# Optimization experiments

Measured on AMD Instinct MI355X. Metric: run time of the kernel, lower is better.

Reference implementation:

```python
import jax, jax.numpy as jnp
import numpy as np

B, S, D = 1, 1024, 4096
NH, NKV, HD = 32, 8, 128
CACHE = 1024


def setup_inputs() -> dict:
    key = jax.random.key(0)
    ks = jax.random.split(key, 9)
    return {
        "hidden_states": jax.random.normal(ks[0], (B, S, D), jnp.float32),
        "freqs_cos": jax.random.uniform(ks[1], (S, HD // 2), jnp.float32),
        "freqs_sin": jax.random.uniform(ks[2], (S, HD // 2), jnp.float32),
        "atten_mask": jnp.zeros((S, CACHE + S), jnp.float32),
        "k_cache": jax.random.normal(ks[3], (B, NKV, HD, CACHE), jnp.float32),
        "v_cache": jax.random.normal(ks[4], (B, NKV, CACHE, HD), jnp.float32),
        "wq": jax.random.normal(ks[5], (NH, HD, D), jnp.float32) * 0.02,
        "wk": jax.random.normal(ks[6], (NKV, HD, D), jnp.float32) * 0.02,
        "wv": jax.random.normal(ks[7], (NKV, HD, D), jnp.float32) * 0.02,
        "wo": jax.random.normal(ks[8], (D, NH * HD), jnp.float32) * 0.02,
    }


def _rope(x, cos, sin):
    # x: [b, s, h, hd]; cos/sin: [s, hd//2]
    half = x.shape[-1] // 2
    xr, xi = x[..., :half], x[..., half:]
    c = cos[None, :, None, :]
    sn = sin[None, :, None, :]
    return jnp.concatenate([xr * c - xi * sn, xr * sn + xi * c], axis=-1)


def reference(hidden_states, freqs_cos, freqs_sin, atten_mask, k_cache, v_cache, wq, wk, wv, wo):
    b, s, d = hidden_states.shape
    nh, hd, _ = wq.shape
    nkv = wk.shape[0]
    g = nh // nkv  # query heads per KV head
    scale = float(hd) ** 0.5

    # projections (equivalent to per-head 1x1 convs)
    q = jnp.einsum("bsd,hed->bshe", hidden_states, wq)   # [b,s,nh,hd]
    k = jnp.einsum("bsd,hed->bshe", hidden_states, wk)   # [b,s,nkv,hd]
    v = jnp.einsum("bsd,hed->bshe", hidden_states, wv)   # [b,s,nkv,hd]

    q = _rope(q, freqs_cos, freqs_sin)
    k = _rope(k, freqs_cos, freqs_sin)

    # concat KV cache: kh [b,nkv,hd,KV], vh [b,nkv,KV,hd]
    kh = jnp.concatenate([k_cache, k.transpose(0, 2, 3, 1)], axis=-1)
    vh = jnp.concatenate([v_cache, v.transpose(0, 2, 1, 3)], axis=2)

    # grouped attention: head i uses kv group i // g
    qg = q.reshape(b, s, nkv, g, hd).transpose(0, 2, 3, 1, 4)  # [b,n,g,s,e]
    scores = jnp.einsum("bngse,bnet->bngst", qg, kh) / scale + atten_mask
    p = jax.nn.softmax(scores, axis=-1)
    yg = jnp.einsum("bngst,bnte->bngse", p, vh)               # [b,n,g,s,e]
    y = yg.transpose(0, 3, 1, 2, 4).reshape(b, s, nh * hd)     # head order n*g+j

    y = jnp.einsum("bsf,df->bsd", y, wo)
    return (y, kh, vh)
```

## Files before the change

kernel.cpp:

```cpp
#include <hip/hip_runtime.h>
#include <hip/hip_bf16.h>
#include <stdint.h>

#define S_LEN 1024
#define D_MODEL 4096
#define NHEAD 32
#define NKV 8
#define HD 128
#define CACHE_T 1024
#define T_TOT 2048
#define NQKV 6144
#define QSCALE 0.08838834764831845f

typedef __attribute__((ext_vector_type(8))) short short8;
typedef __attribute__((ext_vector_type(4))) float floatx4;
typedef __attribute__((ext_vector_type(16))) float floatx16;

__device__ __forceinline__ unsigned short f2bf(float f) {
  union { float f; uint32_t u; } v; v.f = f;
  uint32_t r = v.u + 0x7FFFu + ((v.u >> 16) & 1u);
  return (unsigned short)(r >> 16);
}

__device__ __forceinline__ unsigned pack2bf(float a, float b) {
  union { __hip_bfloat162 h2; unsigned u; } c;
  c.h2 = __float22bfloat162_rn(make_float2(a, b));
  return c.u;
}

__device__ __forceinline__ void gload_lds16(const void* g, void* s) {
  __builtin_amdgcn_global_load_lds((const __attribute__((address_space(1))) void*)g,
                                   (__attribute__((address_space(3))) void*)s, 16, 0, 0);
}

__global__ void convf2b_kernel(const float* __restrict__ in, unsigned short* __restrict__ out, int n8) {
  int stride = gridDim.x * blockDim.x;
  for (int t = blockIdx.x * blockDim.x + threadIdx.x; t < n8; t += stride) {
    int i = t * 8;
    floatx4 a = *(const floatx4*)(in + i);
    floatx4 b = *(const floatx4*)(in + i + 4);
    short8 o;
    o[0] = (short)f2bf(a[0]); o[1] = (short)f2bf(a[1]); o[2] = (short)f2bf(a[2]); o[3] = (short)f2bf(a[3]);
    o[4] = (short)f2bf(b[0]); o[5] = (short)f2bf(b[1]); o[6] = (short)f2bf(b[2]); o[7] = (short)f2bf(b[3]);
    *(short8*)(out + i) = o;
  }
}

__global__ void mask_flag_kernel(const float* __restrict__ m, int n, int* __restrict__ flag) {
  int stride = gridDim.x * blockDim.x;
  bool nz = false;
  for (int i = blockIdx.x * blockDim.x + threadIdx.x; i < n; i += stride)
    nz |= (m[i] != 0.0f);
  if (nz) atomicOr(flag, 1);
}

__global__ __launch_bounds__(256, 3)
void gemm_bf_kernel(const unsigned short* __restrict__ A,
                    const unsigned short* __restrict__ W,
                    float* __restrict__ C,
                    int M, int N, int K, int ldc, int GM)
{
  __shared__ __align__(16) unsigned char As[2][64 * 128];
  __shared__ __align__(16) unsigned char Bs[2][128 * 128];

  const int nwg = gridDim.x;
  int orig = blockIdx.x;
  int wg = (orig & 7) * (nwg >> 3) + (orig >> 3);
  const int mt = wg % GM, nt = wg / GM;
  const int m0 = mt * 64, n0 = nt * 128;

  const int tid = threadIdx.x;
  const int wid = tid >> 6, lane = tid & 63;
  const int g4 = lane >> 4, r16 = lane & 15;
  const int wr = (wid >> 1) * 32, wc = (wid & 1) * 64;

  const int lr = lane >> 3, lc = lane & 7;
  const unsigned short* Arow[2];
  const unsigned short* Wrow[4];
#pragma unroll
  for (int i = 0; i < 2; ++i) {
    int r = (wid * 2 + i) * 8 + lr;
    Arow[i] = A + (size_t)(m0 + r) * K + (lc ^ (r & 7)) * 8;
  }
#pragma unroll
  for (int i = 0; i < 4; ++i) {
    int r = (wid * 4 + i) * 8 + lr;
    Wrow[i] = W + (size_t)(n0 + r) * K + (lc ^ (r & 7)) * 8;
  }

  auto stage = [&](int buf, int kt) {
    const int kb = kt * 64;
#pragma unroll
    for (int i = 0; i < 2; ++i)
      gload_lds16(Arow[i] + kb, &As[buf][(wid * 2 + i) * 1024]);
#pragma unroll
    for (int i = 0; i < 4; ++i)
      gload_lds16(Wrow[i] + kb, &Bs[buf][(wid * 4 + i) * 1024]);
  };

  floatx4 acc[2][4];
#pragma unroll
  for (int m = 0; m < 2; ++m)
#pragma unroll
    for (int n = 0; n < 4; ++n) acc[m][n] = (floatx4){0.f, 0.f, 0.f, 0.f};

  const int NK = K >> 6;
  stage(0, 0);
  __syncthreads();
  int cur = 0;
  for (int kt = 0; kt < NK; ++kt) {
    if (kt + 1 < NK) stage(cur ^ 1, kt + 1);
#pragma unroll
    for (int kk = 0; kk < 2; ++kk) {
      const int kb = kk * 64 + g4 * 16;
      short8 af[2], bf[4];
#pragma unroll
      for (int m = 0; m < 2; ++m) {
        int row = wr + m * 16 + r16;
        af[m] = *(const short8*)(&As[cur][row * 128 + (kb ^ ((row & 7) << 4))]);
      }
#pragma unroll
      for (int n = 0; n < 4; ++n) {
        int row = wc + n * 16 + r16;
        bf[n] = *(const short8*)(&Bs[cur][row * 128 + (kb ^ ((row & 7) << 4))]);
      }
#pragma unroll
      for (int m = 0; m < 2; ++m)
#pragma unroll
        for (int n = 0; n < 4; ++n)
          acc[m][n] = __builtin_amdgcn_mfma_f32_16x16x32_bf16(af[m], bf[n], acc[m][n], 0, 0, 0);
    }
    __syncthreads();
    cur ^= 1;
  }

#pragma unroll
  for (int m = 0; m < 2; ++m)
#pragma unroll
    for (int n = 0; n < 4; ++n)
#pragma unroll
      for (int j = 0; j < 4; ++j)
        C[(size_t)(m0 + wr + m * 16 + g4 * 4 + j) * ldc + (n0 + wc + n * 16 + r16)] = acc[m][n][j];
}

__global__ __launch_bounds__(256, 2)
void gemm_kernel(const unsigned short* __restrict__ A,
                 const float* __restrict__ W0, const float* __restrict__ W1, const float* __restrict__ W2,
                 int n1, int n2,
                 float* __restrict__ C,
                 int M, int N, int K, int GM)
{
  __shared__ __align__(16) unsigned char As[2][128 * 128];
  __shared__ __align__(16) unsigned char Bs[2][128 * 128];

  const int nwg = gridDim.x;
  int orig = blockIdx.x;
  int xcd = orig & 7, loc = orig >> 3;
  int q = nwg >> 3, r = nwg & 7;
  int wg = (xcd < r ? xcd * (q + 1) : r * (q + 1) + (xcd - r) * q) + loc;
  const int mt = wg % GM, nt = wg / GM;
  const int m0 = mt * 128, n0 = nt * 128;

  const int tid = threadIdx.x;
  const int wid = tid >> 6, lane = tid & 63;
  const int g4 = lane >> 4, r16 = lane & 15;
  const int wr = (wid >> 1) * 64, wc = (wid & 1) * 64;

  int srow[4], skc[4];
  const float* wptr[4];
#pragma unroll
  for (int i = 0; i < 4; ++i) {
    int c = tid + 256 * i;
    srow[i] = c >> 3; skc[i] = c & 7;
    int ng = n0 + srow[i];
    wptr[i] = (ng < n1) ? (W0 + (size_t)ng * K)
            : (ng < n2) ? (W1 + (size_t)(ng - n1) * K)
                        : (W2 + (size_t)(ng - n2) * K);
  }

  short8 ar[4]; floatx4 br[8];
  auto load_tile = [&](int kt) {
    int kb = kt * 64;
#pragma unroll
    for (int i = 0; i < 4; ++i) {
      ar[i] = *(const short8*)(A + (size_t)(m0 + srow[i]) * K + kb + skc[i] * 8);
      br[2 * i]     = *(const floatx4*)(wptr[i] + kb + skc[i] * 8);
      br[2 * i + 1] = *(const floatx4*)(wptr[i] + kb + skc[i] * 8 + 4);
    }
  };
  auto write_tile = [&](int buf) {
#pragma unroll
    for (int i = 0; i < 4; ++i) {
      int off = srow[i] * 128 + ((skc[i] * 16) ^ ((srow[i] & 7) << 4));
      *(short8*)(&As[buf][off]) = ar[i];
      short8 bb;
      bb[0] = (short)f2bf(br[2 * i][0]);     bb[1] = (short)f2bf(br[2 * i][1]);
      bb[2] = (short)f2bf(br[2 * i][2]);     bb[3] = (short)f2bf(br[2 * i][3]);
      bb[4] = (short)f2bf(br[2 * i + 1][0]); bb[5] = (short)f2bf(br[2 * i + 1][1]);
      bb[6] = (short)f2bf(br[2 * i + 1][2]); bb[7] = (short)f2bf(br[2 * i + 1][3]);
      *(short8*)(&Bs[buf][off]) = bb;
    }
  };

  floatx4 acc[4][4];
#pragma unroll
  for (int m = 0; m < 4; ++m)
#pragma unroll
    for (int n = 0; n < 4; ++n) acc[m][n] = (floatx4){0.f, 0.f, 0.f, 0.f};

  const int NK = K >> 6;
  load_tile(0);
  write_tile(0);
  __syncthreads();
  int cur = 0;
  for (int kt = 0; kt < NK; ++kt) {
    if (kt + 1 < NK) load_tile(kt + 1);
#pragma unroll
    for (int kk = 0; kk < 2; ++kk) {
      const int kb = kk * 32 + g4 * 8;
      short8 af[4], bfr[4];
#pragma unroll
      for (int m = 0; m < 4; ++m) {
        int row = wr + m * 16 + r16;
        af[m] = *(const short8*)(&As[cur][row * 128 + ((kb * 2) ^ ((row & 7) << 4))]);
      }
#pragma unroll
      for (int n = 0; n < 4; ++n) {
        int row = wc + n * 16 + r16;
        bfr[n] = *(const short8*)(&Bs[cur][row * 128 + ((kb * 2) ^ ((row & 7) << 4))]);
      }
#pragma unroll
      for (int m = 0; m < 4; ++m)
#pragma unroll
        for (int n = 0; n < 4; ++n)
          acc[m][n] = __builtin_amdgcn_mfma_f32_16x16x32_bf16(af[m], bfr[n], acc[m][n], 0, 0, 0);
    }
    if (kt + 1 < NK) write_tile(cur ^ 1);
    __syncthreads();
    cur ^= 1;
  }

#pragma unroll
  for (int m = 0; m < 4; ++m)
#pragma unroll
    for (int n = 0; n < 4; ++n)
#pragma unroll
      for (int j = 0; j < 4; ++j)
        C[(size_t)(m0 + wr + m * 16 + g4 * 4 + j) * N + (n0 + wc + n * 16 + r16)] = acc[m][n][j];
}

__global__ void rope_q_kernel(const float* __restrict__ qkv, const float* __restrict__ fc,
                              const float* __restrict__ fs, unsigned short* __restrict__ qb)
{
  const int s = blockIdx.x, t = threadIdx.x;
  const int head = t >> 3, e0 = (t & 7) * 8;
  const float* base = qkv + (size_t)s * NQKV + head * HD + e0;
  floatx4 xr0 = *(const floatx4*)(base);
  floatx4 xr1 = *(const floatx4*)(base + 4);
  floatx4 xi0 = *(const floatx4*)(base + 64);
  floatx4 xi1 = *(const floatx4*)(base + 68);
  floatx4 c0 = *(const floatx4*)(fc + s * 64 + e0);
  floatx4 c1 = *(const floatx4*)(fc + s * 64 + e0 + 4);
  floatx4 s0 = *(const floatx4*)(fs + s * 64 + e0);
  floatx4 s1 = *(const floatx4*)(fs + s * 64 + e0 + 4);
  short8 outr, outi;
#pragma unroll
  for (int j = 0; j < 4; ++j) {
    outr[j]     = (short)f2bf((xr0[j] * c0[j] - xi0[j] * s0[j]) * QSCALE);
    outr[4 + j] = (short)f2bf((xr1[j] * c1[j] - xi1[j] * s1[j]) * QSCALE);
    outi[j]     = (short)f2bf((xr0[j] * s0[j] + xi0[j] * c0[j]) * QSCALE);
    outi[4 + j] = (short)f2bf((xr1[j] * s1[j] + xi1[j] * c1[j]) * QSCALE);
  }
  unsigned short* ob = qb + (size_t)s * D_MODEL + head * HD + e0;
  *(short8*)ob = outr;
  *(short8*)(ob + 64) = outi;
}

__global__ void prep_k_kernel(const float* __restrict__ qkv, const float* __restrict__ fc,
                              const float* __restrict__ fs, const float* __restrict__ kc,
                              float* __restrict__ kh, unsigned short* __restrict__ khb)
{
  __shared__ __align__(16) unsigned char smem[128 * 65 * 4];
  const int tid = threadIdx.x;

  if (blockIdx.x < 128) {
    float (*T)[65] = (float(*)[65])smem;
    const int b = blockIdx.x;
    const int n = b >> 4, s0 = (b & 15) * 64;
    const int sl = tid >> 2, e0 = (tid & 3) * 16;
    const int s = s0 + sl;
    const float* base = qkv + (size_t)s * NQKV + D_MODEL + n * HD;
    float xr[16], xi[16], cc[16], sn[16];
#pragma unroll
    for (int i = 0; i < 16; i += 4) {
      *(floatx4*)(xr + i) = *(const floatx4*)(base + e0 + i);
      *(floatx4*)(xi + i) = *(const floatx4*)(base + 64 + e0 + i);
      *(floatx4*)(cc + i) = *(const floatx4*)(fc + s * 64 + e0 + i);
      *(floatx4*)(sn + i) = *(const floatx4*)(fs + s * 64 + e0 + i);
    }
    short8 r0, r1, i0, i1;
#pragma unroll
    for (int i = 0; i < 16; ++i) {
      float vr = xr[i] * cc[i] - xi[i] * sn[i];
      float vi = xr[i] * sn[i] + xi[i] * cc[i];
      T[e0 + i][sl] = vr;
      T[64 + e0 + i][sl] = vi;
      unsigned short br = f2bf(vr), bi = f2bf(vi);
      if (i < 8) { r0[i] = (short)br; i0[i] = (short)bi; }
      else       { r1[i - 8] = (short)br; i1[i - 8] = (short)bi; }
    }
    unsigned short* kb = khb + ((size_t)n * T_TOT + CACHE_T + s) * HD;
    *(short8*)(kb + e0) = r0;       *(short8*)(kb + e0 + 8) = r1;
    *(short8*)(kb + 64 + e0) = i0;  *(short8*)(kb + 64 + e0 + 8) = i1;
    __syncthreads();
    const int e = tid >> 1, hf = tid & 1;
    float* dst = kh + ((size_t)n * HD + e) * T_TOT + CACHE_T + s0 + hf * 32;
#pragma unroll
    for (int i = 0; i < 32; i += 4) {
      floatx4 v;
      v[0] = T[e][hf * 32 + i]; v[1] = T[e][hf * 32 + i + 1];
      v[2] = T[e][hf * 32 + i + 2]; v[3] = T[e][hf * 32 + i + 3];
      *(floatx4*)(dst + i) = v;
    }
  } else {
    unsigned short (*T)[72] = (unsigned short(*)[72])smem;
    const int b = blockIdx.x - 128;
    const int n = b >> 5, et = (b >> 4) & 1, tt = b & 15;
    const int e0 = et * 64, t0 = tt * 64;
    const int el = tid >> 2, tc = (tid & 3) * 16;
    const float* src = kc + ((size_t)n * HD + e0 + el) * CACHE_T + t0 + tc;
    float* dst = kh + ((size_t)n * HD + e0 + el) * T_TOT + t0 + tc;
#pragma unroll
    for (int i = 0; i < 16; i += 4) {
      floatx4 v = *(const floatx4*)(src + i);
      *(floatx4*)(dst + i) = v;
      T[tc + i][el] = f2bf(v[0]); T[tc + i + 1][el] = f2bf(v[1]);
      T[tc + i + 2][el] = f2bf(v[2]); T[tc + i + 3][el] = f2bf(v[3]);
    }
    __syncthreads();
    const int tl = tid >> 2, ec = (tid & 3) * 16;
    unsigned short* ob = khb + ((size_t)n * T_TOT + t0 + tl) * HD + e0 + ec;
#pragma unroll
    for (int i = 0; i < 16; i += 8) *(short8*)(ob + i) = *(const short8*)(&T[tl][ec + i]);
  }
}

__global__ void prep_v_kernel(const float* __restrict__ qkv, const float* __restrict__ vc,
                              float* __restrict__ vh, unsigned short* __restrict__ vtb)
{
  __shared__ __align__(16) unsigned short T[128][72];
  const int tid = threadIdx.x;

  if (blockIdx.x < 128) {
    const int b = blockIdx.x;
    const int n = b >> 4, s0 = (b & 15) * 64;
    const int sl = tid >> 2, e0 = (tid & 3) * 32;
    const float* src = qkv + (size_t)(s0 + sl) * NQKV + D_MODEL + NKV * HD + n * HD + e0;
    float* dst = vh + ((size_t)n * T_TOT + CACHE_T + s0 + sl) * HD + e0;
#pragma unroll
    for (int i = 0; i < 32; i += 4) {
      floatx4 v = *(const floatx4*)(src + i);
      *(floatx4*)(dst + i) = v;
      T[e0 + i][sl] = f2bf(v[0]); T[e0 + i + 1][sl] = f2bf(v[1]);
      T[e0 + i + 2][sl] = f2bf(v[2]); T[e0 + i + 3][sl] = f2bf(v[3]);
    }
    __syncthreads();
    const int e = tid >> 1, hf = tid & 1;
    unsigned short* ob = vtb + ((size_t)n * HD + e) * T_TOT + CACHE_T + s0 + hf * 32;
#pragma unroll
    for (int i = 0; i < 32; i += 8) *(short8*)(ob + i) = *(const short8*)(&T[e][hf * 32 + i]);
  } else {
    const int b = blockIdx.x - 128;
    const int n = b >> 4, t0 = (b & 15) * 64;
    const int tl = tid >> 2, e0 = (tid & 3) * 32;
    const float* src = vc + ((size_t)n * CACHE_T + t0 + tl) * HD + e0;
    float* dst = vh + ((size_t)n * T_TOT + t0 + tl) * HD + e0;
#pragma unroll
    for (int i = 0; i < 32; i += 4) {
      floatx4 v = *(const floatx4*)(src + i);
      *(floatx4*)(dst + i) = v;
      T[e0 + i][tl] = f2bf(v[0]); T[e0 + i + 1][tl] = f2bf(v[1]);
      T[e0 + i + 2][tl] = f2bf(v[2]); T[e0 + i + 3][tl] = f2bf(v[3]);
    }
    __syncthreads();
    const int e = tid >> 1, hf = tid & 1;
    unsigned short* ob = vtb + ((size_t)n * HD + e) * T_TOT + t0 + hf * 32;
#pragma unroll
    for (int i = 0; i < 32; i += 8) *(short8*)(ob + i) = *(const short8*)(&T[e][hf * 32 + i]);
  }
}

__global__ __launch_bounds__(256, 2)
void attn_kernel(const unsigned short* __restrict__ Qb, const unsigned short* __restrict__ Kb,
                 const unsigned short* __restrict__ Vb, const float* __restrict__ mask,
                 const int* __restrict__ flag, unsigned short* __restrict__ Ob,
                 float* __restrict__ Upart, float* __restrict__ mlpart, int nsplit)
{
  __shared__ __align__(16) unsigned char KL[2][64 * 256];
  __shared__ __align__(16) unsigned char VL[2][128 * 128];

  const int nwg = gridDim.x;
  int orig = blockIdx.x;
  int wg = (orig & 7) * (nwg >> 3) + (orig >> 3);
  const int per_n = 32 * nsplit;
  const int nkv = wg / per_n;
  const int rem = wg % per_n;
  const int kvs = rem >> 5;
  const int inner = rem & 31;
  const int h = nkv * 4 + (inner >> 3);
  const int qt = inner & 7;
  const int TKV = T_TOT / nsplit;

  const int tid = threadIdx.x, wid = tid >> 6, lane = tid & 63;
  const int l31 = lane & 31, hi = lane >> 5;
  const int qrow = qt * 128 + wid * 32 + l31;
  const bool use_mask = (*flag) != 0;

  short8 qf[8];
#pragma unroll
  for (int c = 0; c < 8; ++c)
    qf[c] = *(const short8*)(Qb + (size_t)qrow * D_MODEL + h * HD + c * 16 + hi * 8);

  floatx16 acc[4];
#pragma unroll
  for (int et = 0; et < 4; ++et)
    acc[et] = (floatx16){0.f,0.f,0.f,0.f,0.f,0.f,0.f,0.f,0.f,0.f,0.f,0.f,0.f,0.f,0.f,0.f};
  float m = -1e30f, l = 0.f;

  const unsigned short* Kbase = Kb + (size_t)nkv * T_TOT * HD + (size_t)kvs * TKV * HD;
  const unsigned short* Vbase = Vb + (size_t)nkv * HD * T_TOT + (size_t)kvs * TKV;

  const unsigned short* kp[4];
  const unsigned short* vp[4];
  int kbase_off[4], vbase_off[4];
#pragma unroll
  for (int i = 0; i < 4; ++i) {
    int krow = wid * 16 + i * 4 + (lane >> 4);
    int kch  = (lane & 15) ^ (krow & 7);
    kp[i] = Kbase + (size_t)krow * HD + kch * 8;
    kbase_off[i] = (wid * 16 + i * 4) * 256;
    int vrow = wid * 32 + i * 8 + (lane >> 3);
    int vch  = (lane & 7) ^ (vrow & 7);
    vp[i] = Vbase + (size_t)vrow * T_TOT + vch * 8;
    vbase_off[i] = (wid * 32 + i * 8) * 128;
  }

#pragma unroll
  for (int i = 0; i < 4; ++i) gload_lds16(kp[i], &KL[0][kbase_off[i]]);
#pragma unroll
  for (int i = 0; i < 4; ++i) gload_lds16(vp[i], &VL[0][vbase_off[i]]);
#pragma unroll
  for (int i = 0; i < 4; ++i) { kp[i] += 64 * HD; vp[i] += 64; }
  __syncthreads();

  int cur = 0;
  for (int t0 = 0; t0 < TKV; t0 += 64) {
    if (t0 + 64 < TKV) {
#pragma unroll
      for (int i = 0; i < 4; ++i) gload_lds16(kp[i], &KL[cur ^ 1][kbase_off[i]]);
#pragma unroll
      for (int i = 0; i < 4; ++i) gload_lds16(vp[i], &VL[cur ^ 1][vbase_off[i]]);
#pragma unroll
      for (int i = 0; i < 4; ++i) { kp[i] += 64 * HD; vp[i] += 64; }
    }

    floatx16 sc[2];
#pragma unroll
    for (int ts = 0; ts < 2; ++ts) {
      sc[ts] = (floatx16){0.f,0.f,0.f,0.f,0.f,0.f,0.f,0.f,0.f,0.f,0.f,0.f,0.f,0.f,0.f,0.f};
      const int krow = ts * 32 + l31;
      const int swz = (krow & 7) << 4;
      const unsigned char* kr = &KL[cur][krow * 256];
#pragma unroll
      for (int c = 0; c < 8; ++c) {
        short8 kf = *(const short8*)(kr + ((c * 32 + hi * 16) ^ swz));
        sc[ts] = __builtin_amdgcn_mfma_f32_32x32x16_bf16(kf, qf[c], sc[ts], 0, 0, 0);
      }
    }

    if (use_mask) {
#pragma unroll
      for (int ts = 0; ts < 2; ++ts)
#pragma unroll
        for (int r = 0; r < 16; ++r) {
          int tg = kvs * TKV + t0 + ts * 32 + (r & 3) + 8 * (r >> 2) + 4 * hi;
          sc[ts][r] += mask[(size_t)qrow * T_TOT + tg];
        }
    }

    float pm = sc[0][0];
#pragma unroll
    for (int r = 1; r < 16; ++r) pm = fmaxf(pm, sc[0][r]);
#pragma unroll
    for (int r = 0; r < 16; ++r) pm = fmaxf(pm, sc[1][r]);
    pm = fmaxf(pm, __shfl_xor(pm, 32));

    if (__any(pm > m + 8.f)) {
      float nm = fmaxf(m, pm);
      float corr = __expf(m - nm);
      m = nm; l *= corr;
#pragma unroll
      for (int r = 0; r < 16; ++r) {
        float cr = __shfl(corr, (r & 3) + 8 * (r >> 2) + 4 * hi);
#pragma unroll
        for (int et = 0; et < 4; ++et) acc[et][r] *= cr;
      }
    }

    unsigned cpk[4][4];
    float ls = 0.f;
#pragma unroll
    for (int ts = 0; ts < 2; ++ts)
#pragma unroll
      for (int i = 0; i < 8; ++i) {
        float plo = __expf(sc[ts][2 * i] - m);
        float phi = __expf(sc[ts][2 * i + 1] - m);
        ls += plo + phi;
        cpk[ts * 2 + (i >> 2)][i & 3] = pack2bf(plo, phi);
      }
    ls += __shfl_xor(ls, 32);
    l += ls;

    short8 pa[4];
#pragma unroll
    for (int tc = 0; tc < 4; ++tc) {
      unsigned s0 = (unsigned)__shfl_xor((int)cpk[tc][0], 32);
      unsigned s1 = (unsigned)__shfl_xor((int)cpk[tc][1], 32);
      unsigned s2 = (unsigned)__shfl_xor((int)cpk[tc][2], 32);
      unsigned s3 = (unsigned)__shfl_xor((int)cpk[tc][3], 32);
      union { unsigned u[4]; short8 v; } fr;
      fr.u[0] = hi ? s2 : cpk[tc][0];
      fr.u[1] = hi ? s3 : cpk[tc][1];
      fr.u[2] = hi ? cpk[tc][2] : s0;
      fr.u[3] = hi ? cpk[tc][3] : s1;
      pa[tc] = fr.v;
    }

#pragma unroll
    for (int et = 0; et < 4; ++et) {
      const int vrow = et * 32 + l31;
      const int swz = (vrow & 7) << 4;
      const unsigned char* vr = &VL[cur][vrow * 128];
#pragma unroll
      for (int tc = 0; tc < 4; ++tc) {
        short8 vf = *(const short8*)(vr + ((tc * 32 + hi * 16) ^ swz));
        acc[et] = __builtin_amdgcn_mfma_f32_32x32x16_bf16(pa[tc], vf, acc[et], 0, 0, 0);
      }
    }
    __syncthreads();
    cur ^= 1;
  }

  if (nsplit == 2) {
    float* Ub = Upart + (size_t)kvs * (NHEAD * S_LEN) * HD;
#pragma unroll
    for (int et = 0; et < 4; ++et)
#pragma unroll
      for (int r = 0; r < 16; ++r) {
        int q = qt * 128 + wid * 32 + (r & 3) + 8 * (r >> 2) + 4 * hi;
        Ub[((size_t)h * S_LEN + q) * HD + et * 32 + l31] = acc[et][r];
      }
    if (lane < 32) {
      float* mlp = mlpart + ((size_t)kvs * (NHEAD * S_LEN) + (size_t)h * S_LEN + qrow) * 2;
      mlp[0] = m; mlp[1] = l;
    }
  } else {
    float inv = 1.0f / l;
#pragma unroll
    for (int et = 0; et < 4; ++et)
#pragma unroll
      for (int r = 0; r < 16; ++r) {
        float ir = __shfl(inv, (r & 3) + 8 * (r >> 2) + 4 * hi);
        int q = qt * 128 + wid * 32 + (r & 3) + 8 * (r >> 2) + 4 * hi;
        Ob[(size_t)q * D_MODEL + h * HD + et * 32 + l31] = f2bf(acc[et][r] * ir);
      }
  }
}

__global__ void attn_combine_kernel(const float* __restrict__ U, const float* __restrict__ ml,
                                    unsigned short* __restrict__ Ob)
{
  const int t = blockIdx.x * 256 + threadIdx.x;
  const int r = t >> 4;
  const int e0 = (t & 15) * 8;
  const float m1 = ml[(size_t)r * 2],                     l1 = ml[(size_t)r * 2 + 1];
  const float m2 = ml[((size_t)(NHEAD * S_LEN) + r) * 2], l2 = ml[((size_t)(NHEAD * S_LEN) + r) * 2 + 1];
  const float M = fmaxf(m1, m2);
  const float a1 = __expf(m1 - M), a2 = __expf(m2 - M);
  const float inv = 1.0f / (l1 * a1 + l2 * a2);
  const float* u1 = U + (size_t)r * HD + e0;
  const float* u2 = U + (size_t)(NHEAD * S_LEN) * HD + (size_t)r * HD + e0;
  floatx4 x1a = *(const floatx4*)u1, x1b = *(const floatx4*)(u1 + 4);
  floatx4 x2a = *(const floatx4*)u2, x2b = *(const floatx4*)(u2 + 4);
  const int s = r & (S_LEN - 1), hh = r >> 10;
  unsigned short* ob = Ob + (size_t)s * D_MODEL + hh * HD + e0;
  short8 o;
#pragma unroll
  for (int k = 0; k < 4; ++k) {
    o[k]     = (short)f2bf((x1a[k] * a1 + x2a[k] * a2) * inv);
    o[4 + k] = (short)f2bf((x1b[k] * a1 + x2b[k] * a2) * inv);
  }
  *(short8*)ob = o;
}

extern "C" void kernel_launch(void* const* d_in, const int* in_sizes, int n_in,
                              void* d_out, int out_size, void* d_ws, size_t ws_size,
                              hipStream_t stream)
{
  const float* hs   = (const float*)d_in[0];
  const float* fc   = (const float*)d_in[1];
  const float* fs   = (const float*)d_in[2];
  const float* mask = (const float*)d_in[3];
  const float* kc   = (const float*)d_in[4];
  const float* vc   = (const float*)d_in[5];
  const float* wq   = (const float*)d_in[6];
  const float* wk   = (const float*)d_in[7];
  const float* wv   = (const float*)d_in[8];
  const float* wo   = (const float*)d_in[9];

  float* y  = (float*)d_out;
  float* kh = y + (size_t)S_LEN * D_MODEL;
  float* vh = kh + (size_t)NKV * HD * T_TOT;

  char* ws = (char*)d_ws;
  unsigned short* hs_b   = (unsigned short*)ws;
  float* qkv             = (float*)(ws + 8388608u);
  unsigned short* attn_o = (unsigned short*)(ws + 8388608u);
  unsigned short* khb    = (unsigned short*)(ws + 33554432u);
  unsigned short* vtb    = (unsigned short*)(ws + 37748736u);
  int* flag              = (int*)(ws + 41943040u);
  unsigned short* slotW  = (unsigned short*)(ws + 41943296u);

  const size_t base = 41943296ull;
  const bool big = ws_size >= base + 50331648ull;
  const bool mid = ws_size >= base + 33554432ull;
  const int nsplit = (ws_size >= base + 34078720ull) ? 2 : 1;
  float* Upart  = (float*)(ws + base);
  float* mlpart = (float*)(ws + base + 33554432u);

  hipMemsetAsync(flag, 0, 4, stream);
  mask_flag_kernel<<<256, 256, 0, stream>>>(mask, S_LEN * T_TOT, flag);
  convf2b_kernel<<<2048, 256, 0, stream>>>(hs, hs_b, S_LEN * D_MODEL / 8);

  if (big) {
    convf2b_kernel<<<2048, 256, 0, stream>>>(wq, slotW, NHEAD * HD * D_MODEL / 8);
    convf2b_kernel<<<2048, 256, 0, stream>>>(wk, slotW + (size_t)4096 * 4096, NKV * HD * D_MODEL / 8);
    convf2b_kernel<<<2048, 256, 0, stream>>>(wv, slotW + (size_t)5120 * 4096, NKV * HD * D_MODEL / 8);
    gemm_bf_kernel<<<768, 256, 0, stream>>>(hs_b, slotW, qkv, 1024, 6144, 4096, 6144, 16);
  } else if (mid) {
    convf2b_kernel<<<2048, 256, 0, stream>>>(wk, slotW, NKV * HD * D_MODEL / 8);
    convf2b_kernel<<<2048, 256, 0, stream>>>(wv, slotW + (size_t)1024 * 4096, NKV * HD * D_MODEL / 8);
    gemm_bf_kernel<<<256, 256, 0, stream>>>(hs_b, slotW, qkv + 4096, 1024, 2048, 4096, 6144, 16);
    convf2b_kernel<<<2048, 256, 0, stream>>>(wq, slotW, NHEAD * HD * D_MODEL / 8);
    gemm_bf_kernel<<<512, 256, 0, stream>>>(hs_b, slotW, qkv, 1024, 4096, 4096, 6144, 16);
  } else {
    gemm_kernel<<<384, 256, 0, stream>>>(hs_b, wq, wk, wv, 4096, 5120, qkv, 1024, 6144, 4096, 8);
  }

  rope_q_kernel<<<1024, 256, 0, stream>>>(qkv, fc, fs, hs_b);
  prep_k_kernel<<<384, 256, 0, stream>>>(qkv, fc, fs, kc, kh, khb);
  prep_v_kernel<<<256, 256, 0, stream>>>(qkv, vc, vh, vtb);

  attn_kernel<<<256 * nsplit, 256, 0, stream>>>(hs_b, khb, vtb, mask, flag, attn_o,
                                                Upart, mlpart, nsplit);
  if (nsplit == 2)
    attn_combine_kernel<<<2048, 256, 0, stream>>>(Upart, mlpart, attn_o);

  if (mid) {
    convf2b_kernel<<<2048, 256, 0, stream>>>(wo, slotW, D_MODEL * D_MODEL / 8);
    gemm_bf_kernel<<<512, 256, 0, stream>>>(attn_o, slotW, y, 1024, 4096, 4096, 4096, 16);
  } else {
    gemm_kernel<<<256, 256, 0, stream>>>(attn_o, wo, wo, wo, 1 << 29, 1 << 29, y, 1024, 4096, 4096, 8);
  }
}
```

Before: 266.1 us.

## Fuse fp32 weight conversion into QKV GEMM with direct-to-LDS fp32 loads

Adds a GEMM kernel that loads fp32 Wq/Wk/Wv tiles straight into LDS and converts them to bf16 while building MFMA operands. It replaces the separate weight-conversion passes and the bf16 GEMM for the QKV projection. This removes the extra write and re-read of a bf16 weight copy. In exchange it doubles LDS traffic for W, does per-iteration packing work in the inner loop, and lowers occupancy to 2 blocks per CU.

```diff
diff --git a/kernel.cpp b/kernel.cpp
--- a/kernel.cpp
+++ b/kernel.cpp
@@ -52,6 +52,110 @@
   for (int i = blockIdx.x * blockDim.x + threadIdx.x; i < n; i += stride)
     nz |= (m[i] != 0.0f);
   if (nz) atomicOr(flag, 1);
+}
+
+__global__ __launch_bounds__(256, 2)
+void gemm_fw2_kernel(const unsigned short* __restrict__ A,
+                     const float* __restrict__ W0, const float* __restrict__ W1, const float* __restrict__ W2,
+                     int n1, int n2,
+                     float* __restrict__ C,
+                     int M, int N, int K, int ldc, int GM)
+{
+  __shared__ __align__(16) unsigned char As[2][64 * 128];
+  __shared__ __align__(16) unsigned char Wf[2][128 * 256];
+
+  const int nwg = gridDim.x;
+  int orig = blockIdx.x;
+  int wg = (orig & 7) * (nwg >> 3) + (orig >> 3);
+  const int mt = wg % GM, nt = wg / GM;
+  const int m0 = mt * 64, n0 = nt * 128;
+
+  const int tid = threadIdx.x;
+  const int wid = tid >> 6, lane = tid & 63;
+  const int g4 = lane >> 4, r16 = lane & 15;
+  const int wr = (wid >> 1) * 32, wc = (wid & 1) * 64;
+
+  const int lr = lane >> 3, lc = lane & 7;
+  const unsigned short* Arow[2];
+#pragma unroll
+  for (int i = 0; i < 2; ++i) {
+    int r = (wid * 2 + i) * 8 + lr;
+    Arow[i] = A + (size_t)(m0 + r) * K + (lc ^ (r & 7)) * 8;
+  }
+
+  const float* Wsrc[8];
+#pragma unroll
+  for (int j = 0; j < 8; ++j) {
+    int r = j * 16 + (tid >> 4);
+    int pos = tid & 15;
+    int ng = n0 + r;
+    const float* p = (ng < n1) ? (W0 + (size_t)ng * K)
+                   : (ng < n2) ? (W1 + (size_t)(ng - n1) * K)
+                               : (W2 + (size_t)(ng - n2) * K);
+    Wsrc[j] = p + (pos ^ (r & 15)) * 4;
+  }
+
+  auto stage = [&](int buf, int kt) {
+    const int kb = kt * 64;
+#pragma unroll
+    for (int i = 0; i < 2; ++i)
+      gload_lds16(Arow[i] + kb, &As[buf][(wid * 2 + i) * 1024]);
+#pragma unroll
+    for (int j = 0; j < 8; ++j)
+      gload_lds16(Wsrc[j] + kb, &Wf[buf][j * 4096 + tid * 16]);
+  };
+
+  floatx4 acc[2][4];
+#pragma unroll
+  for (int m = 0; m < 2; ++m)
+#pragma unroll
+    for (int n = 0; n < 4; ++n) acc[m][n] = (floatx4){0.f, 0.f, 0.f, 0.f};
+
+  const int NK = K >> 6;
+  stage(0, 0);
+  __syncthreads();
+  int cur = 0;
+  for (int kt = 0; kt < NK; ++kt) {
+    if (kt + 1 < NK) stage(cur ^ 1, kt + 1);
+#pragma unroll
+    for (int kk = 0; kk < 2; ++kk) {
+      short8 af[2], bf[4];
+#pragma unroll
+      for (int m = 0; m < 2; ++m) {
+        int row = wr + m * 16 + r16;
+        af[m] = *(const short8*)(&As[cur][row * 128 + ((kk * 64 + g4 * 16) ^ ((row & 7) << 4))]);
+      }
+      const int cc = kk * 8 + g4 * 2;
+#pragma unroll
+      for (int n = 0; n < 4; ++n) {
+        int row = wc + n * 16 + r16;
+        const unsigned char* wrp = &Wf[cur][row * 256];
+        floatx4 w0 = *(const floatx4*)(wrp + ((cc ^ (row & 15)) << 4));
+        floatx4 w1 = *(const floatx4*)(wrp + (((cc + 1) ^ (row & 15)) << 4));
+        union { unsigned u[4]; short8 v; } pk;
+        pk.u[0] = pack2bf(w0[0], w0[1]);
+        pk.u[1] = pack2bf(w0[2], w0[3]);
+        pk.u[2] = pack2bf(w1[0], w1[1]);
+        pk.u[3] = pack2bf(w1[2], w1[3]);
+        bf[n] = pk.v;
+      }
+#pragma unroll
+      for (int m = 0; m < 2; ++m)
+#pragma unroll
+        for (int n = 0; n < 4; ++n)
+          acc[m][n] = __builtin_amdgcn_mfma_f32_16x16x32_bf16(af[m], bf[n], acc[m][n], 0, 0, 0);
+    }
+    __syncthreads();
+    cur ^= 1;
+  }
+
+#pragma unroll
+  for (int m = 0; m < 2; ++m)
+#pragma unroll
+    for (int n = 0; n < 4; ++n)
+#pragma unroll
+      for (int j = 0; j < 4; ++j)
+        C[(size_t)(m0 + wr + m * 16 + g4 * 4 + j) * ldc + (n0 + wc + n * 16 + r16)] = acc[m][n][j];
 }
 
 __global__ __launch_bounds__(256, 3)
@@ -632,7 +736,6 @@
   unsigned short* slotW  = (unsigned short*)(ws + 41943296u);
 
   const size_t base = 41943296ull;
-  const bool big = ws_size >= base + 50331648ull;
   const bool mid = ws_size >= base + 33554432ull;
   const int nsplit = (ws_size >= base + 34078720ull) ? 2 : 1;
   float* Upart  = (float*)(ws + base);
@@ -642,20 +745,8 @@
   mask_flag_kernel<<<256, 256, 0, stream>>>(mask, S_LEN * T_TOT, flag);
   convf2b_kernel<<<2048, 256, 0, stream>>>(hs, hs_b, S_LEN * D_MODEL / 8);
 
-  if (big) {
-    convf2b_kernel<<<2048, 256, 0, stream>>>(wq, slotW, NHEAD * HD * D_MODEL / 8);
-    convf2b_kernel<<<2048, 256, 0, stream>>>(wk, slotW + (size_t)4096 * 4096, NKV * HD * D_MODEL / 8);
-    convf2b_kernel<<<2048, 256, 0, stream>>>(wv, slotW + (size_t)5120 * 4096, NKV * HD * D_MODEL / 8);
-    gemm_bf_kernel<<<768, 256, 0, stream>>>(hs_b, slotW, qkv, 1024, 6144, 4096, 6144, 16);
-  } else if (mid) {
-    convf2b_kernel<<<2048, 256, 0, stream>>>(wk, slotW, NKV * HD * D_MODEL / 8);
-    convf2b_kernel<<<2048, 256, 0, stream>>>(wv, slotW + (size_t)1024 * 4096, NKV * HD * D_MODEL / 8);
-    gemm_bf_kernel<<<256, 256, 0, stream>>>(hs_b, slotW, qkv + 4096, 1024, 2048, 4096, 6144, 16);
-    convf2b_kernel<<<2048, 256, 0, stream>>>(wq, slotW, NHEAD * HD * D_MODEL / 8);
-    gemm_bf_kernel<<<512, 256, 0, stream>>>(hs_b, slotW, qkv, 1024, 4096, 4096, 6144, 16);
-  } else {
-    gemm_kernel<<<384, 256, 0, stream>>>(hs_b, wq, wk, wv, 4096, 5120, qkv, 1024, 6144, 4096, 8);
-  }
+  gemm_fw2_kernel<<<768, 256, 0, stream>>>(hs_b, wq, wk, wv, 4096, 5120, qkv,
+                                           1024, 6144, 4096, 6144, 16);
 
   rope_q_kernel<<<1024, 256, 0, stream>>>(qkv, fc, fs, hs_b);
   prep_k_kernel<<<384, 256, 0, stream>>>(qkv, fc, fs, kc, kh, khb);
```

Result: slower. 362.0 us (+36.0%).
